# Kernel tuning notes

Hardware: AMD Instinct MI355X
Metric: run time of the kernel (lower is better)

Reference implementation:

```python
import jax, jax.numpy as jnp
import numpy as np

N = 100000
E = 1600000
IN_CH, HID_CH, OUT_CH = 128, 64, 32


def setup_inputs() -> dict:
    key = jax.random.key(0)
    ks = jax.random.split(key, 6)
    x = jax.random.normal(ks[0], (N, IN_CH), dtype=jnp.float32)
    ei = jax.random.randint(ks[1], (2, E), 0, N, dtype=jnp.int64)
    W1 = jax.random.normal(ks[2], (IN_CH, HID_CH), dtype=jnp.float32) * 0.05
    b1 = jax.random.normal(ks[3], (HID_CH,), dtype=jnp.float32) * 0.05
    W2 = jax.random.normal(ks[4], (HID_CH, OUT_CH), dtype=jnp.float32) * 0.05
    b2 = jax.random.normal(ks[5], (OUT_CH,), dtype=jnp.float32) * 0.05
    return {"x": x, "ei": ei, "W1": W1, "b1": b1, "W2": W2, "b2": b2}


def gcn_layer(x, sa, da, n):
    # degree with self-loops already appended in sa/da
    deg = jax.ops.segment_sum(jnp.ones((sa.shape[0],), x.dtype), da, num_segments=n)
    prod = deg[sa] * deg[da]
    norm = jnp.where(prod > 0, jax.lax.rsqrt(prod), 0.0)  # (deg_s*deg_d)^-0.5, inf->0
    msg = x[sa] * norm[:, None]            # [E+N, C] gather + scale
    return jax.ops.segment_sum(msg, da, num_segments=n)  # scatter_add


def reference(x, ei, W1, b1, W2, b2):
    n = x.shape[0]
    loop = jnp.arange(n, dtype=ei.dtype)
    sa = jnp.concatenate([ei[0], loop])
    da = jnp.concatenate([ei[1], loop])
    h = gcn_layer(x @ W1 + b1, sa, da, n)
    h = jax.nn.relu(h)
    # dropout: eval mode (training=False) -> identity
    return gcn_layer(h @ W2 + b2, sa, da, n)
```

## Files before the change

kernel.cpp:

```cpp
#include <hip/hip_runtime.h>

#define NN 100000
#define NE 1600000
#define IN_CH 128
#define HID_CH 64
#define OUT_CH 32
#define NB2 98
#define CHUNKA 8192

typedef unsigned short ushort_t;
typedef _Float16 half2_t __attribute__((ext_vector_type(2)));

__device__ inline ushort_t f2bf(float f) {
    union { float f; unsigned u; } v; v.f = f;
    unsigned r = v.u + 0x7fff + ((v.u >> 16) & 1);
    return (ushort_t)(r >> 16);
}
__device__ inline float blo(unsigned u) {
    union { unsigned x; float f; } v; v.x = u << 16; return v.f;
}
__device__ inline float bhi(unsigned u) {
    union { unsigned x; float f; } v; v.x = u & 0xffff0000u; return v.f;
}
__device__ inline unsigned pkh(float a, float b) {
    union { half2_t h; unsigned u; } v;
    v.h[0] = (_Float16)a; v.h[1] = (_Float16)b;
    return v.u;
}
__device__ inline half2_t u2h(unsigned u) {
    union { unsigned u; half2_t h; } v; v.u = u; return v.h;
}
__device__ inline float fdot2(unsigned a, unsigned b, float c) {
#if __has_builtin(__builtin_amdgcn_fdot2)
    return __builtin_amdgcn_fdot2(u2h(a), u2h(b), c, false);
#else
    half2_t ha = u2h(a), hb = u2h(b);
    return c + (float)ha[0] * (float)hb[0] + (float)ha[1] * (float)hb[1];
#endif
}

__global__ __launch_bounds__(256) void k_bhist(const int* __restrict__ da,
                                               int* __restrict__ bcnt) {
    __shared__ int hist[4][NB2];
    int t = threadIdx.x, w = t >> 6;
    for (int i = t; i < 4 * NB2; i += 256) ((int*)hist)[i] = 0;
    __syncthreads();
    int base = blockIdx.x * CHUNKA;
    for (int i = 0; i < CHUNKA; i += 256) {
        int e = base + i + t;
        if (e < NE) atomicAdd(&hist[w][da[e] >> 10], 1);
    }
    __syncthreads();
    if (t < NB2) {
        int c = hist[0][t] + hist[1][t] + hist[2][t] + hist[3][t];
        if (c) atomicAdd(&bcnt[t], c);
    }
}

__global__ __launch_bounds__(128) void k_bscan(const int* __restrict__ bcnt,
                                               int* __restrict__ bbase,
                                               int* __restrict__ bcur,
                                               int* __restrict__ rowptr) {
    __shared__ int lds[128];
    int t = threadIdx.x;
    int v = (t < NB2) ? bcnt[t] : 0;
    lds[t] = v;
    __syncthreads();
    for (int off = 1; off < 128; off <<= 1) {
        int x = (t >= off) ? lds[t - off] : 0;
        __syncthreads();
        lds[t] += x;
        __syncthreads();
    }
    int excl = lds[t] - v;
    if (t < NB2) { bbase[t] = excl; bcur[t] = excl; }
    if (t == 0) { bbase[NB2] = NE; rowptr[NN] = NE; }
}

__global__ __launch_bounds__(256) void k_bfill(const int* __restrict__ sa,
                                               const int* __restrict__ da,
                                               int* __restrict__ bcur,
                                               unsigned* __restrict__ ebuf) {
    __shared__ int hist[4][NB2];
    __shared__ int lcur[NB2];
    int t = threadIdx.x, w = t >> 6;
    for (int i = t; i < 4 * NB2; i += 256) ((int*)hist)[i] = 0;
    __syncthreads();
    int base = blockIdx.x * CHUNKA;
    for (int i = 0; i < CHUNKA; i += 256) {
        int e = base + i + t;
        if (e < NE) atomicAdd(&hist[w][da[e] >> 10], 1);
    }
    __syncthreads();
    if (t < NB2) {
        int c = hist[0][t] + hist[1][t] + hist[2][t] + hist[3][t];
        lcur[t] = c ? atomicAdd(&bcur[t], c) : 0;
    }
    __syncthreads();
    for (int i = 0; i < CHUNKA; i += 256) {
        int e = base + i + t;
        if (e < NE) {
            int d = da[e];
            int p = atomicAdd(&lcur[d >> 10], 1);
            ebuf[p] = ((unsigned)sa[e] << 10) | (unsigned)(d & 1023);
        }
    }
}

__global__ __launch_bounds__(1024) void k_bfine(const unsigned* __restrict__ ebuf,
                                                const int* __restrict__ bbase,
                                                int* __restrict__ rowptr,
                                                float* __restrict__ rs,
                                                int* __restrict__ col) {
    __shared__ int cnt[1024];
    __shared__ int cur[1024];
    __shared__ int scn[1024];
    int b = blockIdx.x, t = threadIdx.x;
    int nb = NN - b * 1024; if (nb > 1024) nb = 1024;
    int beg = bbase[b], end = bbase[b + 1];
    cnt[t] = 0;
    __syncthreads();
    for (int i = beg + t; i < end; i += 1024) atomicAdd(&cnt[ebuf[i] & 1023], 1);
    __syncthreads();
    int v = cnt[t];
    scn[t] = v;
    __syncthreads();
    for (int off = 1; off < 1024; off <<= 1) {
        int x = (t >= off) ? scn[t - off] : 0;
        __syncthreads();
        scn[t] += x;
        __syncthreads();
    }
    int excl = scn[t] - v;
    if (t < nb) {
        rowptr[b * 1024 + t] = beg + excl;
        rs[b * 1024 + t] = rsqrtf((float)(v + 1));
        cur[t] = beg + excl;
    }
    __syncthreads();
    for (int i = beg + t; i < end; i += 1024) {
        unsigned p = ebuf[i];
        int pos = atomicAdd(&cur[p & 1023], 1);
        col[pos] = (int)(p >> 10);
    }
}

#define SWZU1(n, k2) ((n) * 64 + ((k2) ^ ((((n) & 7)) << 2)))
#define SWZ2(n, k) ((n) * 64 + ((k) ^ ((((n) & 7)) << 2)))

__global__ __launch_bounds__(256, 4) void k_gemm1(
    const float* __restrict__ x, const float* __restrict__ W1,
    const float* __restrict__ b1, const float* __restrict__ rs,
    ushort_t* __restrict__ xsb) {
    __shared__ unsigned xth[64 * 64];
    __shared__ unsigned w1h[64 * 64];
    int t = threadIdx.x;
    int base = blockIdx.x * 64;

#pragma unroll
    for (int i = 0; i < 8; ++i) {
        int flat = i * 1024 + t * 4;
        int node = flat >> 7, k0 = flat & 127;
        int gn = base + node;
        float4 v = make_float4(0.f, 0.f, 0.f, 0.f);
        if (gn < NN) v = *(const float4*)(x + (size_t)gn * IN_CH + k0);
        uint2 pk;
        pk.x = pkh(v.x, v.y);
        pk.y = pkh(v.z, v.w);
        *(uint2*)&xth[SWZU1(node, k0 >> 1)] = pk;
    }
#pragma unroll
    for (int i = 0; i < 16; ++i) {
        int idx = i * 256 + t;
        int k2 = idx >> 6, c = idx & 63;
        float f0 = W1[(2 * k2) * 64 + c];
        float f1 = W1[(2 * k2 + 1) * 64 + c];
        w1h[idx] = pkh(f0, f1);
    }
    __syncthreads();

    int tn = t & 15, tc = t >> 4;
    int c0 = tc * 4;
    float acc[4][4];
#pragma unroll
    for (int a = 0; a < 4; ++a)
#pragma unroll
        for (int b = 0; b < 4; ++b) acc[a][b] = 0.f;

    for (int k2 = 0; k2 < 64; k2 += 2) {
        uint2 xu[4];
#pragma unroll
        for (int jn = 0; jn < 4; ++jn)
            xu[jn] = *(uint2*)&xth[SWZU1(tn + jn * 16, k2)];
        uint4 w0 = *(uint4*)&w1h[(k2 + 0) * 64 + c0];
        uint4 w1 = *(uint4*)&w1h[(k2 + 1) * 64 + c0];
        unsigned wq0[4] = {w0.x, w0.y, w0.z, w0.w};
        unsigned wq1[4] = {w1.x, w1.y, w1.z, w1.w};
#pragma unroll
        for (int jn = 0; jn < 4; ++jn)
#pragma unroll
            for (int jc = 0; jc < 4; ++jc) {
                acc[jn][jc] = fdot2(xu[jn].x, wq0[jc], acc[jn][jc]);
                acc[jn][jc] = fdot2(xu[jn].y, wq1[jc], acc[jn][jc]);
            }
    }

    float4 bb = *(const float4*)&b1[c0];
#pragma unroll
    for (int jn = 0; jn < 4; ++jn) {
        int gn = base + tn + jn * 16;
        if (gn < NN) {
            float r = rs[gn];
            uint2 pk;
            pk.x = (unsigned)f2bf((acc[jn][0] + bb.x) * r) |
                   ((unsigned)f2bf((acc[jn][1] + bb.y) * r) << 16);
            pk.y = (unsigned)f2bf((acc[jn][2] + bb.z) * r) |
                   ((unsigned)f2bf((acc[jn][3] + bb.w) * r) << 16);
            *(uint2*)&xsb[(size_t)gn * HID_CH + c0] = pk;
        }
    }
}

#define ADD8(v) do { \
    a0 += blo((v).x); a1 += bhi((v).x); a2 += blo((v).y); a3 += bhi((v).y); \
    a4 += blo((v).z); a5 += bhi((v).z); a6 += blo((v).w); a7 += bhi((v).w); } while (0)

__global__ __launch_bounds__(256) void k_agg1(
    const int* __restrict__ rowptr, const int* __restrict__ col,
    const ushort_t* __restrict__ xsb, const float* __restrict__ rs,
    ushort_t* __restrict__ hb) {
    int gid = blockIdx.x * blockDim.x + threadIdx.x;
    int n = gid >> 6;
    if (n >= NN) return;
    int lane = threadIdx.x & 63;
    int g = lane >> 3;
    unsigned c0 = (unsigned)(lane & 7) * 8;
    int beg = rowptr[n], end = rowptr[n + 1];

    float a0 = 0.f, a1 = 0.f, a2 = 0.f, a3 = 0.f;
    float a4 = 0.f, a5 = 0.f, a6 = 0.f, a7 = 0.f;
    if (g == 0) {
        uint4 sv = *(const uint4*)&xsb[(unsigned)n * 64u + c0];
        ADD8(sv);
    }

    int i = beg;
    for (; i + 16 <= end; i += 16) {
        int s0 = col[i + g];
        int s1 = col[i + 8 + g];
        uint4 v0 = *(const uint4*)&xsb[(unsigned)s0 * 64u + c0];
        uint4 v1 = *(const uint4*)&xsb[(unsigned)s1 * 64u + c0];
        ADD8(v0);
        ADD8(v1);
    }
    if (i + 8 <= end) {
        int s0 = col[i + g];
        uint4 v0 = *(const uint4*)&xsb[(unsigned)s0 * 64u + c0];
        ADD8(v0);
        i += 8;
    }
    int r = end - i;
    if (g < r) {
        int s0 = col[i + g];
        uint4 v0 = *(const uint4*)&xsb[(unsigned)s0 * 64u + c0];
        ADD8(v0);
    }

#pragma unroll
    for (int m = 8; m <= 32; m <<= 1) {
        a0 += __shfl_xor(a0, m); a1 += __shfl_xor(a1, m);
        a2 += __shfl_xor(a2, m); a3 += __shfl_xor(a3, m);
        a4 += __shfl_xor(a4, m); a5 += __shfl_xor(a5, m);
        a6 += __shfl_xor(a6, m); a7 += __shfl_xor(a7, m);
    }

    if (g == 0) {
        float rn = rs[n];
        uint4 pk;
        pk.x = (unsigned)f2bf(fmaxf(a0 * rn, 0.f)) |
               ((unsigned)f2bf(fmaxf(a1 * rn, 0.f)) << 16);
        pk.y = (unsigned)f2bf(fmaxf(a2 * rn, 0.f)) |
               ((unsigned)f2bf(fmaxf(a3 * rn, 0.f)) << 16);
        pk.z = (unsigned)f2bf(fmaxf(a4 * rn, 0.f)) |
               ((unsigned)f2bf(fmaxf(a5 * rn, 0.f)) << 16);
        pk.w = (unsigned)f2bf(fmaxf(a6 * rn, 0.f)) |
               ((unsigned)f2bf(fmaxf(a7 * rn, 0.f)) << 16);
        *(uint4*)&hb[(unsigned)n * 64u + c0] = pk;
    }
}

__global__ __launch_bounds__(256) void k_gemm2(
    const ushort_t* __restrict__ hb, const float* __restrict__ W2,
    const float* __restrict__ b2, const float* __restrict__ rs,
    ushort_t* __restrict__ ysb) {
    __shared__ float ht[64 * 64];
    __shared__ float w2s[64 * 32];
    int t = threadIdx.x;
    int base = blockIdx.x * 64;

#pragma unroll
    for (int i = 0; i < 8; ++i) {
        int uidx = i * 256 + t;
        int node = uidx >> 5, k2 = uidx & 31;
        int gn = base + node;
        unsigned u = 0;
        if (gn < NN) u = *(const unsigned*)&hb[(size_t)gn * HID_CH + k2 * 2];
        float2 f; f.x = blo(u); f.y = bhi(u);
        *(float2*)&ht[SWZ2(node, k2 * 2)] = f;
    }
#pragma unroll
    for (int i = 0; i < 2; ++i) {
        int flat = i * 1024 + t * 4;
        *(float4*)&w2s[flat] = *(const float4*)(W2 + flat);
    }
    __syncthreads();

    int tn = t & 15, tc = t >> 4;
    int c0 = tc * 2;
    float acc[4][2];
#pragma unroll
    for (int a = 0; a < 4; ++a) { acc[a][0] = 0.f; acc[a][1] = 0.f; }

    for (int k0 = 0; k0 < 64; k0 += 4) {
        float xq[4][4], wq[4][2];
#pragma unroll
        for (int j = 0; j < 4; ++j)
            *(float2*)&wq[j][0] = *(float2*)&w2s[(k0 + j) * 32 + c0];
#pragma unroll
        for (int jn = 0; jn < 4; ++jn)
            *(float4*)&xq[jn][0] = *(float4*)&ht[SWZ2(tn + jn * 16, k0)];
#pragma unroll
        for (int jn = 0; jn < 4; ++jn)
#pragma unroll
            for (int j = 0; j < 4; ++j) {
                acc[jn][0] = fmaf(xq[jn][j], wq[j][0], acc[jn][0]);
                acc[jn][1] = fmaf(xq[jn][j], wq[j][1], acc[jn][1]);
            }
    }

    float2 bb = *(const float2*)&b2[c0];
#pragma unroll
    for (int jn = 0; jn < 4; ++jn) {
        int gn = base + tn + jn * 16;
        if (gn < NN) {
            float r = rs[gn];
            unsigned pk = (unsigned)f2bf((acc[jn][0] + bb.x) * r) |
                          ((unsigned)f2bf((acc[jn][1] + bb.y) * r) << 16);
            *(unsigned*)&ysb[(size_t)gn * OUT_CH + c0] = pk;
        }
    }
}

__global__ __launch_bounds__(256) void k_agg2(
    const int* __restrict__ rowptr, const int* __restrict__ col,
    const ushort_t* __restrict__ ysb, const float* __restrict__ rs,
    float* __restrict__ out) {
    int gid = blockIdx.x * blockDim.x + threadIdx.x;
    int n = gid >> 6;
    if (n >= NN) return;
    int lane = threadIdx.x & 63;
    int g = lane >> 2;
    unsigned c0 = (unsigned)(lane & 3) * 8;
    int beg = rowptr[n], end = rowptr[n + 1];

    float a0 = 0.f, a1 = 0.f, a2 = 0.f, a3 = 0.f;
    float a4 = 0.f, a5 = 0.f, a6 = 0.f, a7 = 0.f;
    if (g == 0) {
        uint4 sv = *(const uint4*)&ysb[(unsigned)n * 32u + c0];
        ADD8(sv);
    }

    int i = beg;
    for (; i + 16 <= end; i += 16) {
        int s0 = col[i + g];
        uint4 v0 = *(const uint4*)&ysb[(unsigned)s0 * 32u + c0];
        ADD8(v0);
    }
    int r = end - i;
    if (g < r) {
        int s0 = col[i + g];
        uint4 v0 = *(const uint4*)&ysb[(unsigned)s0 * 32u + c0];
        ADD8(v0);
    }

#pragma unroll
    for (int m = 4; m <= 32; m <<= 1) {
        a0 += __shfl_xor(a0, m); a1 += __shfl_xor(a1, m);
        a2 += __shfl_xor(a2, m); a3 += __shfl_xor(a3, m);
        a4 += __shfl_xor(a4, m); a5 += __shfl_xor(a5, m);
        a6 += __shfl_xor(a6, m); a7 += __shfl_xor(a7, m);
    }

    if (g == 0) {
        float rn = rs[n];
        float4 o0, o1;
        o0.x = a0 * rn; o0.y = a1 * rn; o0.z = a2 * rn; o0.w = a3 * rn;
        o1.x = a4 * rn; o1.y = a5 * rn; o1.z = a6 * rn; o1.w = a7 * rn;
        *(float4*)&out[(size_t)n * OUT_CH + c0] = o0;
        *(float4*)&out[(size_t)n * OUT_CH + c0 + 4] = o1;
    }
}

extern "C" void kernel_launch(void* const* d_in, const int* in_sizes, int n_in,
                              void* d_out, int out_size, void* d_ws, size_t ws_size,
                              hipStream_t stream) {
    const float* x  = (const float*)d_in[0];
    const int*   ei = (const int*)d_in[1];
    const float* W1 = (const float*)d_in[2];
    const float* b1 = (const float*)d_in[3];
    const float* W2 = (const float*)d_in[4];
    const float* b2 = (const float*)d_in[5];
    const int* sa = ei;
    const int* da = ei + NE;

    char* ws = (char*)d_ws;
    size_t off = 0;
    auto alloc = [&](size_t bytes) {
        void* p = ws + off;
        off += (bytes + 255) & ~(size_t)255;
        return p;
    };
    int*      bcnt   = (int*)alloc((size_t)NB2 * 4);
    int*      bbase  = (int*)alloc((size_t)(NB2 + 1) * 4);
    int*      bcur   = (int*)alloc((size_t)NB2 * 4);
    int*      rowptr = (int*)alloc((size_t)(NN + 1) * 4);
    float*    rs     = (float*)alloc((size_t)NN * 4);
    unsigned* ebuf   = (unsigned*)alloc((size_t)NE * 4);
    int*      col    = (int*)alloc((size_t)NE * 4);
    ushort_t* xsb    = (ushort_t*)alloc((size_t)NN * HID_CH * 2);
    ushort_t* hb     = (ushort_t*)alloc((size_t)NN * HID_CH * 2);
    ushort_t* ysb    = (ushort_t*)alloc((size_t)NN * OUT_CH * 2);
    float*    outp   = (float*)d_out;

    const int B = 256;
    const int NBLKA = (NE + CHUNKA - 1) / CHUNKA;
    hipMemsetAsync(bcnt, 0, (size_t)NB2 * 4, stream);
    k_bhist<<<NBLKA, 256, 0, stream>>>(da, bcnt);
    k_bscan<<<1, 128, 0, stream>>>(bcnt, bbase, bcur, rowptr);
    k_bfill<<<NBLKA, 256, 0, stream>>>(sa, da, bcur, ebuf);
    k_bfine<<<NB2, 1024, 0, stream>>>(ebuf, bbase, rowptr, rs, col);

    const int NBLK_GEMM = (NN + 63) / 64;
    k_gemm1<<<NBLK_GEMM, 256, 0, stream>>>(x, W1, b1, rs, xsb);
    k_agg1<<<(NN * 64 + B - 1) / B, B, 0, stream>>>(rowptr, col, xsb, rs, hb);
    k_gemm2<<<NBLK_GEMM, 256, 0, stream>>>(hb, W2, b2, rs, ysb);
    k_agg2<<<(NN * 64 + B - 1) / B, B, 0, stream>>>(rowptr, col, ysb, rs, outp);
}
```

Before: 222.4 us.

## Reuse per-block histograms in fill and split fine bucketing across four blocks

k_bhist now stores each block's per-bucket counts in a workspace array, so k_bfill no longer re-reads the destination indices to rebuild its histogram. k_bfine changes from 98 blocks of 1024 threads to 392 blocks of 256 threads. Each block re-counts the whole bucket but only writes the rowptr, rs and col entries for its quarter of the 1024 destinations. This spreads the CSR build over more CUs, at the cost of four redundant reads of each bucket's edges and a small extra buffer.

```diff
diff --git a/kernel.cpp b/kernel.cpp
--- a/kernel.cpp
+++ b/kernel.cpp
@@ -7,6 +7,7 @@
 #define OUT_CH 32
 #define NB2 98
 #define CHUNKA 8192
+#define NBLKA ((NE + CHUNKA - 1) / CHUNKA)
 
 typedef unsigned short ushort_t;
 typedef _Float16 half2_t __attribute__((ext_vector_type(2)));
@@ -40,7 +41,8 @@
 }
 
 __global__ __launch_bounds__(256) void k_bhist(const int* __restrict__ da,
-                                               int* __restrict__ bcnt) {
+                                               int* __restrict__ bcnt,
+                                               int* __restrict__ bhall) {
     __shared__ int hist[4][NB2];
     int t = threadIdx.x, w = t >> 6;
     for (int i = t; i < 4 * NB2; i += 256) ((int*)hist)[i] = 0;
@@ -53,6 +55,7 @@
     __syncthreads();
     if (t < NB2) {
         int c = hist[0][t] + hist[1][t] + hist[2][t] + hist[3][t];
+        bhall[blockIdx.x * NB2 + t] = c;
         if (c) atomicAdd(&bcnt[t], c);
     }
 }
@@ -79,24 +82,17 @@
 
 __global__ __launch_bounds__(256) void k_bfill(const int* __restrict__ sa,
                                                const int* __restrict__ da,
+                                               const int* __restrict__ bhall,
                                                int* __restrict__ bcur,
                                                unsigned* __restrict__ ebuf) {
-    __shared__ int hist[4][NB2];
     __shared__ int lcur[NB2];
-    int t = threadIdx.x, w = t >> 6;
-    for (int i = t; i < 4 * NB2; i += 256) ((int*)hist)[i] = 0;
+    int t = threadIdx.x;
+    if (t < NB2) {
+        int c = bhall[blockIdx.x * NB2 + t];
+        lcur[t] = c ? atomicAdd(&bcur[t], c) : 0;
+    }
     __syncthreads();
     int base = blockIdx.x * CHUNKA;
-    for (int i = 0; i < CHUNKA; i += 256) {
-        int e = base + i + t;
-        if (e < NE) atomicAdd(&hist[w][da[e] >> 10], 1);
-    }
-    __syncthreads();
-    if (t < NB2) {
-        int c = hist[0][t] + hist[1][t] + hist[2][t] + hist[3][t];
-        lcur[t] = c ? atomicAdd(&bcur[t], c) : 0;
-    }
-    __syncthreads();
     for (int i = 0; i < CHUNKA; i += 256) {
         int e = base + i + t;
         if (e < NE) {
@@ -107,41 +103,54 @@
     }
 }
 
-__global__ __launch_bounds__(1024) void k_bfine(const unsigned* __restrict__ ebuf,
-                                                const int* __restrict__ bbase,
-                                                int* __restrict__ rowptr,
-                                                float* __restrict__ rs,
-                                                int* __restrict__ col) {
+__global__ __launch_bounds__(256) void k_bfine(const unsigned* __restrict__ ebuf,
+                                               const int* __restrict__ bbase,
+                                               int* __restrict__ rowptr,
+                                               float* __restrict__ rs,
+                                               int* __restrict__ col) {
     __shared__ int cnt[1024];
-    __shared__ int cur[1024];
-    __shared__ int scn[1024];
+    __shared__ int scn[256];
+    __shared__ int cur[256];
     int b = blockIdx.x, t = threadIdx.x;
-    int nb = NN - b * 1024; if (nb > 1024) nb = 1024;
-    int beg = bbase[b], end = bbase[b + 1];
-    cnt[t] = 0;
-    __syncthreads();
-    for (int i = beg + t; i < end; i += 1024) atomicAdd(&cnt[ebuf[i] & 1023], 1);
-    __syncthreads();
-    int v = cnt[t];
-    scn[t] = v;
-    __syncthreads();
-    for (int off = 1; off < 1024; off <<= 1) {
+    int B = b >> 2, slice = b & 3;
+    int beg = bbase[B], end = bbase[B + 1];
+    *(int4*)&cnt[t * 4] = make_int4(0, 0, 0, 0);
+    __syncthreads();
+    for (int i = beg + t; i < end; i += 256) atomicAdd(&cnt[ebuf[i] & 1023], 1);
+    __syncthreads();
+    int4 v4 = *(int4*)&cnt[t * 4];
+    int s = v4.x + v4.y + v4.z + v4.w;
+    scn[t] = s;
+    __syncthreads();
+    for (int off = 1; off < 256; off <<= 1) {
         int x = (t >= off) ? scn[t - off] : 0;
         __syncthreads();
         scn[t] += x;
         __syncthreads();
     }
-    int excl = scn[t] - v;
-    if (t < nb) {
-        rowptr[b * 1024 + t] = beg + excl;
-        rs[b * 1024 + t] = rsqrtf((float)(v + 1));
-        cur[t] = beg + excl;
-    }
-    __syncthreads();
-    for (int i = beg + t; i < end; i += 1024) {
-        unsigned p = ebuf[i];
-        int pos = atomicAdd(&cur[p & 1023], 1);
-        col[pos] = (int)(p >> 10);
+    int excl = scn[t] - s;
+    if ((t >> 6) == slice) {
+        int p0 = excl;
+        int p1 = p0 + v4.x;
+        int p2 = p1 + v4.y;
+        int p3 = p2 + v4.z;
+        int dlo = t * 4;
+        int n = B * 1024 + dlo;
+        int ci = dlo - slice * 256;
+        if (n + 0 < NN) { rowptr[n + 0] = beg + p0; rs[n + 0] = rsqrtf((float)(v4.x + 1)); cur[ci + 0] = beg + p0; }
+        if (n + 1 < NN) { rowptr[n + 1] = beg + p1; rs[n + 1] = rsqrtf((float)(v4.y + 1)); cur[ci + 1] = beg + p1; }
+        if (n + 2 < NN) { rowptr[n + 2] = beg + p2; rs[n + 2] = rsqrtf((float)(v4.z + 1)); cur[ci + 2] = beg + p2; }
+        if (n + 3 < NN) { rowptr[n + 3] = beg + p3; rs[n + 3] = rsqrtf((float)(v4.w + 1)); cur[ci + 3] = beg + p3; }
+    }
+    __syncthreads();
+    int slo = slice * 256;
+    for (int i = beg + t; i < end; i += 256) {
+        unsigned w = ebuf[i];
+        int dlo = (int)(w & 1023);
+        if ((dlo >> 8) == slice) {
+            int pos = atomicAdd(&cur[dlo - slo], 1);
+            col[pos] = (int)(w >> 10);
+        }
     }
 }
 
@@ -423,6 +432,7 @@
     int*      bcnt   = (int*)alloc((size_t)NB2 * 4);
     int*      bbase  = (int*)alloc((size_t)(NB2 + 1) * 4);
     int*      bcur   = (int*)alloc((size_t)NB2 * 4);
+    int*      bhall  = (int*)alloc((size_t)NBLKA * NB2 * 4);
     int*      rowptr = (int*)alloc((size_t)(NN + 1) * 4);
     float*    rs     = (float*)alloc((size_t)NN * 4);
     unsigned* ebuf   = (unsigned*)alloc((size_t)NE * 4);
@@ -433,12 +443,11 @@
     float*    outp   = (float*)d_out;
 
     const int B = 256;
-    const int NBLKA = (NE + CHUNKA - 1) / CHUNKA;
     hipMemsetAsync(bcnt, 0, (size_t)NB2 * 4, stream);
-    k_bhist<<<NBLKA, 256, 0, stream>>>(da, bcnt);
+    k_bhist<<<NBLKA, 256, 0, stream>>>(da, bcnt, bhall);
     k_bscan<<<1, 128, 0, stream>>>(bcnt, bbase, bcur, rowptr);
-    k_bfill<<<NBLKA, 256, 0, stream>>>(sa, da, bcur, ebuf);
-    k_bfine<<<NB2, 1024, 0, stream>>>(ebuf, bbase, rowptr, rs, col);
+    k_bfill<<<NBLKA, 256, 0, stream>>>(sa, da, bhall, bcur, ebuf);
+    k_bfine<<<NB2 * 4, 256, 0, stream>>>(ebuf, bbase, rowptr, rs, col);
 
     const int NBLK_GEMM = (NN + 63) / 64;
     k_gemm1<<<NBLK_GEMM, 256, 0, stream>>>(x, W1, b1, rs, xsb);
```

New measurement: 242.3 us. +9.0%, slower.
